# Kernel optimization log

Hardware: AMD Instinct MI355X
Metric: run time of the kernel (lower is better)

Reference implementation:

```python
import jax, jax.numpy as jnp
import numpy as np

NP_, NA_ = 50000, 20000
D_IN, D_HID, D_OUT = 128, 128, 64
E_W, E_C, E_R = 250000, 500000, 250000


def setup_inputs() -> dict:
    key = jax.random.key(0)
    ks = jax.random.split(key, 14)
    s_in = 1.0 / np.sqrt(D_IN)
    s_h = 1.0 / np.sqrt(D_HID)
    return {
        "x_paper": jax.random.normal(ks[0], (NP_, D_IN), jnp.float32),
        "x_author": jax.random.normal(ks[1], (NA_, D_IN), jnp.float32),
        "Wl1": jax.random.normal(ks[2], (3, D_HID, D_IN), jnp.float32) * s_in,
        "bl1": jax.random.normal(ks[3], (3, D_HID), jnp.float32) * 0.01,
        "Wr1": jax.random.normal(ks[4], (3, D_HID, D_IN), jnp.float32) * s_in,
        "Wl2": jax.random.normal(ks[5], (3, D_OUT, D_HID), jnp.float32) * s_h,
        "bl2": jax.random.normal(ks[6], (3, D_OUT), jnp.float32) * 0.01,
        "Wr2": jax.random.normal(ks[7], (3, D_OUT, D_HID), jnp.float32) * s_h,
        "writes_src": jax.random.randint(ks[8], (E_W,), 0, NA_),
        "writes_dst": jax.random.randint(ks[9], (E_W,), 0, NP_),
        "cites_src": jax.random.randint(ks[10], (E_C,), 0, NP_),
        "cites_dst": jax.random.randint(ks[11], (E_C,), 0, NP_),
        "rev_src": jax.random.randint(ks[12], (E_R,), 0, NP_),
        "rev_dst": jax.random.randint(ks[13], (E_R,), 0, NA_),
    }


def _sage(x_src, x_dst, src, dst, Wl, bl, Wr, n_dst):
    # PyG SAGEConv(aggr='mean'): lin_l(mean_j x_src[j]) + lin_r(x_dst)
    agg = jax.ops.segment_sum(x_src[src], dst, num_segments=n_dst)
    cnt = jax.ops.segment_sum(jnp.ones_like(dst, dtype=x_src.dtype), dst,
                              num_segments=n_dst)
    agg = agg / jnp.maximum(cnt, 1.0)[:, None]  # degree-0 nodes -> 0 (PyG scatter-mean)
    return agg @ Wl.T + bl + x_dst @ Wr.T


def reference(x_paper, x_author, Wl1, bl1, Wr1, Wl2, bl2, Wr2,
              writes_src, writes_dst, cites_src, cites_dst, rev_src, rev_dst):
    def hetero_layer(xp, xa, Wl, bl, Wr):
        # HeteroConv(aggr='mean'): average per-relation outputs per dst node type
        op = 0.5 * (_sage(xa, xp, writes_src, writes_dst, Wl[0], bl[0], Wr[0], NP_)
                    + _sage(xp, xp, cites_src, cites_dst, Wl[1], bl[1], Wr[1], NP_))
        oa = _sage(xp, xa, rev_src, rev_dst, Wl[2], bl[2], Wr[2], NA_)
        return op, oa

    hp, ha = hetero_layer(x_paper, x_author, Wl1, bl1, Wr1)
    hp, ha = jax.nn.relu(hp), jax.nn.relu(ha)  # norm_type='none', dropout eval-mode
    hp, _ = hetero_layer(hp, ha, Wl2, bl2, Wr2)
    return hp  # logits for category='paper', [NP_, D_OUT]
```

## Files before the change

kernel.cpp:

```cpp
#include <hip/hip_runtime.h>

#define NP 50000
#define NA 20000
#define E_W 250000
#define E_C 500000
#define E_R 250000
#define E_TOT (E_W + E_C + E_R)
#define CAP 48
#define RBLK 4096
#define NSEG 245
#define PNODES 15000
#define CHK 500
#define NCH 30
#define NBIN 240

typedef __attribute__((ext_vector_type(8))) short short8;
typedef __attribute__((ext_vector_type(4))) float floatx4;
typedef __attribute__((ext_vector_type(2))) float floatx2;

__device__ __forceinline__ unsigned short f2bf(float f) {
    unsigned u = __float_as_uint(f);
    return (unsigned short)((u + 0x7FFFu + ((u >> 16) & 1u)) >> 16);
}
__device__ __forceinline__ float bflo(unsigned v) { return __uint_as_float(v << 16); }
__device__ __forceinline__ float bfhi(unsigned v) { return __uint_as_float(v & 0xFFFF0000u); }

__device__ __forceinline__ int node_idx(int node) {
    if (node < 2 * NP) {
        int rel1 = node >= NP;
        int d = node - (rel1 ? NP : 0);
        int p2 = d / 6250;
        return p2 * PNODES + (d - p2 * 6250) + (rel1 ? 6250 : 0);
    }
    int d = node - 2 * NP;
    int p2 = d / 2500;
    return p2 * PNODES + 12500 + (d - p2 * 2500);
}

__device__ __forceinline__ int frag_off(int NT, int j, int n, int k) {
    int t = n >> 4, ln = n & 15;
    int kb = k >> 5, q = (k >> 3) & 3, r = k & 7;
    return (((j * NT + t) * 4 + kb) * 64 + q * 16 + ln) * 8 + r;
}

__device__ __forceinline__ void prep_body(
    int idx,
    const float* __restrict__ xp, const float* __restrict__ xa,
    const float* __restrict__ Wl1, const float* __restrict__ Wr1,
    const float* __restrict__ Wl2, const float* __restrict__ Wr2,
    const float* __restrict__ bl1, const float* __restrict__ bl2,
    unsigned short* __restrict__ xpb, unsigned short* __restrict__ xab,
    unsigned* __restrict__ xp8, unsigned* __restrict__ xa8,
    unsigned short* __restrict__ Wp1, unsigned short* __restrict__ Wa1,
    unsigned short* __restrict__ Wt2, unsigned short* __restrict__ Wr2s,
    float* __restrict__ bias_p1, float* __restrict__ bias_a1,
    float* __restrict__ bias_p2) {
    const int n4p = NP * 32, n4a = NA * 32;
    if (idx < n4p + n4a) {
        const float* s; unsigned short* d; unsigned* d8; int i = idx;
        if (i < n4p) { s = xp; d = xpb; d8 = xp8; }
        else { s = xa; d = xab; d8 = xa8; i -= n4p; }
        float4 v = ((const float4*)s)[i];
        ushort4 u;
        u.x = f2bf(v.x); u.y = f2bf(v.y); u.z = f2bf(v.z); u.w = f2bf(v.w);
        ((ushort4*)d)[i] = u;
        int w = __builtin_amdgcn_cvt_pk_fp8_f32(v.x, v.y, 0, false);
        w = __builtin_amdgcn_cvt_pk_fp8_f32(v.z, v.w, w, true);
        d8[i] = (unsigned)w;
        return;
    }
    int j = idx - (n4p + n4a);
    if (j < 49152) {
        int jj = j >> 14, rem = j & 16383, n = rem >> 7, k = rem & 127;
        float v = (jj == 0)   ? 0.5f * Wl1[rem]
                  : (jj == 1) ? 0.5f * Wl1[16384 + rem]
                              : 0.5f * (Wr1[rem] + Wr1[16384 + rem]);
        Wp1[frag_off(8, jj, n, k)] = f2bf(v);
    } else if (j < 81920) {
        int i2 = j - 49152;
        int jj = i2 >> 14, rem = i2 & 16383, n = rem >> 7, k = rem & 127;
        float v = (jj == 0) ? Wl1[2 * 16384 + rem] : Wr1[2 * 16384 + rem];
        Wa1[frag_off(8, jj, n, k)] = f2bf(v);
    } else if (j < 98304) {
        int i2 = j - 81920;
        int jj = i2 >> 13, rem = i2 & 8191, n = rem >> 7, k = rem & 127;
        float v = 0.5f * Wl2[jj * 8192 + rem];
        Wt2[frag_off(4, jj, n, k)] = f2bf(v);
    } else if (j < 106496) {
        int i2 = j - 98304;
        int n = i2 >> 7, k = i2 & 127;
        float v = 0.5f * (Wr2[i2] + Wr2[8192 + i2]);
        Wr2s[frag_off(4, 0, n, k)] = f2bf(v);
    } else if (j < 106496 + 320) {
        int b = j - 106496;
        if (b < 128) bias_p1[b] = 0.5f * (bl1[b] + bl1[128 + b]);
        else if (b < 256) bias_a1[b - 128] = bl1[256 + b - 128];
        else bias_p2[b - 256] = 0.5f * (bl2[b - 256] + bl2[64 + b - 256]);
    }
}

__device__ __forceinline__ void edge_bin(
    int e, const int* __restrict__ w_src, const int* __restrict__ w_dst,
    const int* __restrict__ c_src, const int* __restrict__ c_dst,
    const int* __restrict__ r_src, const int* __restrict__ r_dst,
    int& bin, int& sub, int& src) {
    bool isC = (e >= E_W) & (e < E_W + E_C);
    bool isR = e >= E_W + E_C;
    const int* db = isR ? r_dst : (isC ? c_dst : w_dst);
    const int* sb = isR ? r_src : (isC ? c_src : w_src);
    int idx = e - (isC ? E_W : 0) - (isR ? (E_W + E_C) : 0);
    int d = db[idx];
    src = sb[idx];
    int p, local;
    if (isR) { p = d / 2500; local = 12500 + d - p * 2500; }
    else { p = d / 6250; local = (d - p * 6250) + (isC ? 6250 : 0); }
    int ch = local / CHK;
    bin = p * NCH + ch;
    sub = local - ch * CHK;
}

__device__ __forceinline__ void route_body(
    int bid, const int* __restrict__ w_src, const int* __restrict__ w_dst,
    const int* __restrict__ c_src, const int* __restrict__ c_dst,
    const int* __restrict__ r_src, const int* __restrict__ r_dst,
    unsigned* __restrict__ seg, int* __restrict__ segoff, int* __restrict__ segcnt,
    int* cnt_s, int* base_s, int* cur_s) {
    int tid = threadIdx.x, lane = tid & 63;
    for (int k = tid; k < NBIN; k += 256) cnt_s[k] = 0;
    __syncthreads();
#pragma unroll 4
    for (int u = 0; u < 16; ++u) {
        int e = bid * RBLK + u * 256 + tid;
        if (e < E_TOT) {
            int bin, sub, src;
            edge_bin(e, w_src, w_dst, c_src, c_dst, r_src, r_dst, bin, sub, src);
            atomicAdd(&cnt_s[bin], 1);
        }
    }
    __syncthreads();
    if (tid < 64) {
        int v[4], tot = 0;
#pragma unroll
        for (int q = 0; q < 4; ++q) {
            int k = tid * 4 + q;
            v[q] = (k < NBIN) ? cnt_s[k] : 0;
            tot += v[q];
        }
        int sc = tot;
#pragma unroll
        for (int ofs = 1; ofs < 64; ofs <<= 1) {
            int t = __shfl_up(sc, ofs, 64);
            if (lane >= ofs) sc += t;
        }
        int run = sc - tot;
#pragma unroll
        for (int q = 0; q < 4; ++q) {
            int k = tid * 4 + q;
            if (k < NBIN) { base_s[k] = run; run += v[q]; }
        }
    }
    __syncthreads();
    for (int k = tid; k < NBIN; k += 256) {
        segoff[bid * NBIN + k] = base_s[k];
        segcnt[bid * NBIN + k] = cnt_s[k];
        cur_s[k] = base_s[k];
    }
    __syncthreads();
    unsigned* segb = seg + (size_t)bid * RBLK;
#pragma unroll 4
    for (int u = 0; u < 16; ++u) {
        int e = bid * RBLK + u * 256 + tid;
        if (e < E_TOT) {
            int bin, sub, src;
            edge_bin(e, w_src, w_dst, c_src, c_dst, r_src, r_dst, bin, sub, src);
            int pos = atomicAdd(&cur_s[bin], 1);
            segb[pos] = (unsigned)src | ((unsigned)sub << 16);
        }
    }
}

__global__ __launch_bounds__(256) void route_prep(
    const float* xp, const float* xa, const float* Wl1, const float* Wr1,
    const float* Wl2, const float* Wr2, const float* bl1, const float* bl2,
    unsigned short* xpb, unsigned short* xab, unsigned* xp8, unsigned* xa8,
    unsigned short* Wp1, unsigned short* Wa1, unsigned short* Wt2, unsigned short* Wr2s,
    float* bias_p1, float* bias_a1, float* bias_p2,
    const int* w_src, const int* w_dst, const int* c_src, const int* c_dst,
    const int* r_src, const int* r_dst,
    unsigned* seg, int* segoff, int* segcnt) {
    __shared__ int cnt_s[NBIN], base_s[NBIN], cur_s[NBIN];
    if ((int)blockIdx.x < NSEG)
        route_body(blockIdx.x, w_src, w_dst, c_src, c_dst, r_src, r_dst,
                   seg, segoff, segcnt, cnt_s, base_s, cur_s);
    else
        prep_body((blockIdx.x - NSEG) * 256 + threadIdx.x, xp, xa, Wl1, Wr1, Wl2, Wr2,
                  bl1, bl2, xpb, xab, xp8, xa8, Wp1, Wa1, Wt2, Wr2s,
                  bias_p1, bias_a1, bias_p2);
}

__global__ __launch_bounds__(256) void fill2c(
    const unsigned* __restrict__ seg, const int* __restrict__ segoff,
    const int* __restrict__ segcnt, int* __restrict__ cnt,
    unsigned short* __restrict__ csr) {
    __shared__ unsigned short rows[CHK * CAP];
    __shared__ int cursor[CHK];
    __shared__ int offs[NSEG], cnts[NSEG];
    int k = blockIdx.x, tid = threadIdx.x;
    for (int s = tid; s < NSEG; s += 256) {
        offs[s] = segoff[s * NBIN + k];
        cnts[s] = segcnt[s * NBIN + k];
    }
    for (int l = tid; l < CHK; l += 256) cursor[l] = 0;
    __syncthreads();
    int grp = tid >> 4, gl = tid & 15;
    for (int s = grp; s < NSEG; s += 16) {
        int n = cnts[s];
        const unsigned* sp = seg + (size_t)s * RBLK + offs[s];
        for (int i = gl; i < n; i += 16) {
            unsigned v = sp[i];
            int sub = v >> 16, src = v & 0xFFFFu;
            int pos = atomicAdd(&cursor[sub], 1);
            if (pos < CAP) rows[sub * CAP + pos] = (unsigned short)src;
        }
    }
    __syncthreads();
    int p = k / NCH, ch = k - p * NCH;
    int gbase = p * PNODES + ch * CHK;
    for (int l = tid; l < CHK; l += 256) cnt[gbase + l] = cursor[l];
    const unsigned* rU = (const unsigned*)rows;
    unsigned* cU = (unsigned*)csr + (size_t)gbase * (CAP / 2);
    for (int i = tid; i < CHK * (CAP / 2); i += 256) cU[i] = rU[i];
}

__global__ void agg_pad(const unsigned* __restrict__ s0, unsigned short* __restrict__ d0,
                        const unsigned* __restrict__ s1, unsigned short* __restrict__ d1,
                        const unsigned* __restrict__ s2, unsigned short* __restrict__ d2,
                        const int* __restrict__ cnt, const unsigned short* __restrict__ csr) {
    int g = blockIdx.x * 8 + (threadIdx.x >> 5);
    int lane = threadIdx.x & 63;
    int sl = lane & 31, hw = lane & 32;
    const unsigned* sp; unsigned short* dst; int node, dummy;
    if (g < NP) { sp = s0; dst = d0; node = g; dummy = NA; }
    else if (g < 2 * NP) { sp = s1; dst = d1; node = g - NP; dummy = NP; }
    else if (g < 2 * NP + NA) { sp = s2; dst = d2; node = g - 2 * NP; dummy = NP; }
    else return;
    int idx = node_idx(g);
    int deg = cnt[idx];
    int degc = deg < CAP ? deg : CAP;
    const unsigned short* row = csr + (size_t)idx * CAP;
    int ei0 = (sl < degc) ? (int)row[sl] : dummy;
    int ei1 = (32 + sl < degc) ? (int)row[32 + sl] : dummy;
    int degw = degc;
    int other = __shfl_xor(degw, 32, 64);
    if (other > degw) degw = other;
    float a0 = 0.f, a1 = 0.f, a2 = 0.f, a3 = 0.f;
    float b0 = 0.f, b1 = 0.f, b2 = 0.f, b3 = 0.f;
    for (int i = 0; i < degw; i += 8) {
        unsigned v[8];
#pragma unroll
        for (int u = 0; u < 8; ++u) {
            int ii = i + u;
            int esrc = (ii < 32) ? ei0 : ei1;
            int qq = __shfl(esrc, hw | (ii & 31), 64);
            qq = (ii < degc) ? qq : dummy;
            v[u] = sp[(size_t)qq * 32 + sl];
        }
#pragma unroll
        for (int u = 0; u < 8; ++u) {
            floatx2 lo = __builtin_amdgcn_cvt_pk_f32_fp8(v[u], false);
            floatx2 hi = __builtin_amdgcn_cvt_pk_f32_fp8(v[u], true);
            if (u & 1) { b0 += lo.x; b1 += lo.y; b2 += hi.x; b3 += hi.y; }
            else       { a0 += lo.x; a1 += lo.y; a2 += hi.x; a3 += hi.y; }
        }
    }
    float scl = deg > 0 ? 1.f / (float)deg : 0.f;
    float r0 = (a0 + b0) * scl, r1 = (a1 + b1) * scl;
    float r2 = (a2 + b2) * scl, r3 = (a3 + b3) * scl;
    unsigned wlo = ((unsigned)f2bf(r1) << 16) | (unsigned)f2bf(r0);
    unsigned whi = ((unsigned)f2bf(r3) << 16) | (unsigned)f2bf(r2);
    ((uint2*)dst)[(size_t)node * 32 + sl] = make_uint2(wlo, whi);
}

__global__ void agg2(const unsigned short* __restrict__ ta, const unsigned short* __restrict__ tp,
                     const int* __restrict__ cnt, const unsigned short* __restrict__ csr,
                     const float* __restrict__ sp_in, const float* __restrict__ bias_p2,
                     float* __restrict__ out) {
    int node = blockIdx.x * 8 + (threadIdx.x >> 5);
    if (node >= NP) return;
    int lane = threadIdx.x & 63;
    int sl = lane & 31;
    int hw = lane & 32;
    int p2 = node / 6250;
    int base = p2 * PNODES + (node - p2 * 6250);
    float r0 = 0.f, r1 = 0.f;
#pragma unroll
    for (int rel = 0; rel < 2; ++rel) {
        int dummy = (rel == 0) ? NA : NP;
        const unsigned* sp = (const unsigned*)((rel == 0) ? ta : tp);
        int idx = base + (rel ? 6250 : 0);
        int deg = cnt[idx];
        int degc = deg < CAP ? deg : CAP;
        const unsigned short* row = csr + (size_t)idx * CAP;
        int ei0 = (sl < degc) ? (int)row[sl] : dummy;
        int ei1 = (32 + sl < degc) ? (int)row[32 + sl] : dummy;
        int degw = degc;
        int other = __shfl_xor(degw, 32, 64);
        if (other > degw) degw = other;
        float s0 = 0.f, s1 = 0.f, t0 = 0.f, t1 = 0.f;
        for (int i = 0; i < degw; i += 8) {
            unsigned v[8];
#pragma unroll
            for (int u = 0; u < 8; ++u) {
                int ii = i + u;
                int esrc = (ii < 32) ? ei0 : ei1;
                int qq = __shfl(esrc, hw | (ii & 31), 64);
                qq = (ii < degc) ? qq : dummy;
                v[u] = sp[(size_t)qq * 32 + sl];
            }
#pragma unroll
            for (int u = 0; u < 8; ++u) {
                if (u & 1) { t0 += bflo(v[u]); t1 += bfhi(v[u]); }
                else       { s0 += bflo(v[u]); s1 += bfhi(v[u]); }
            }
        }
        float scl = deg > 0 ? 1.f / (float)deg : 0.f;
        r0 += (s0 + t0) * scl; r1 += (s1 + t1) * scl;
    }
    float2 spv = ((const float2*)sp_in)[(size_t)node * 32 + sl];
    float2 bv = ((const float2*)bias_p2)[sl];
    ((float2*)out)[(size_t)node * 32 + sl] =
        make_float2(r0 + spv.x + bv.x, r1 + spv.y + bv.y);
}

template <int J, bool SP>
__device__ __forceinline__ void l1_core(
    const unsigned short* __restrict__ A0, const unsigned short* __restrict__ A1,
    const unsigned short* __restrict__ A2, const unsigned short* __restrict__ Wf,
    const float* __restrict__ bias,
    const unsigned short* __restrict__ Wt, unsigned short* __restrict__ tout,
    const unsigned short* __restrict__ Wsp, float* __restrict__ spout,
    unsigned short (*hT)[136], int M, int blk) {
    int tid = threadIdx.x;
    int wave = tid >> 6, lane = tid & 63;
    int ln = lane & 15, quad = lane >> 4;
    int row = blk * 64 + wave * 16 + ln;
    int rowc = row < M ? row : M - 1;
    const unsigned short* As[3] = {A0, A1, A2};
    floatx4 acc[8];
#pragma unroll
    for (int t = 0; t < 8; ++t) acc[t] = (floatx4){0.f, 0.f, 0.f, 0.f};
#pragma unroll
    for (int j = 0; j < J; ++j) {
        const unsigned short* A = As[j] + (long)rowc * 128 + quad * 8;
        const unsigned short* Wj = Wf + j * (128 * 128) + lane * 8;
#pragma unroll
        for (int kb = 0; kb < 4; ++kb) {
            short8 af = *(const short8*)(A + kb * 32);
#pragma unroll
            for (int t = 0; t < 8; ++t) {
                short8 bf = *(const short8*)(Wj + (t * 4 + kb) * 512);
                acc[t] = __builtin_amdgcn_mfma_f32_16x16x32_bf16(af, bf, acc[t], 0, 0, 0);
            }
        }
    }
    int orow0 = blk * 64 + wave * 16 + quad * 4;
    int lrow0 = wave * 16 + quad * 4;
#pragma unroll
    for (int t = 0; t < 8; ++t) {
        int col = t * 16 + ln;
        float bv = bias[col];
#pragma unroll
        for (int r = 0; r < 4; ++r) {
            float v = fmaxf(acc[t][r] + bv, 0.f);
            hT[lrow0 + r][col] = f2bf(v);
        }
    }
    __syncthreads();
    floatx4 tacc[4], sacc[4];
#pragma unroll
    for (int t = 0; t < 4; ++t) {
        tacc[t] = (floatx4){0.f, 0.f, 0.f, 0.f};
        sacc[t] = (floatx4){0.f, 0.f, 0.f, 0.f};
    }
#pragma unroll
    for (int kb = 0; kb < 4; ++kb) {
        short8 af = *(const short8*)&hT[wave * 16 + ln][quad * 8 + kb * 32];
#pragma unroll
        for (int t = 0; t < 4; ++t) {
            short8 bf = *(const short8*)(Wt + (t * 4 + kb) * 512 + lane * 8);
            tacc[t] = __builtin_amdgcn_mfma_f32_16x16x32_bf16(af, bf, tacc[t], 0, 0, 0);
            if (SP) {
                short8 bs = *(const short8*)(Wsp + (t * 4 + kb) * 512 + lane * 8);
                sacc[t] = __builtin_amdgcn_mfma_f32_16x16x32_bf16(af, bs, sacc[t], 0, 0, 0);
            }
        }
    }
#pragma unroll
    for (int t = 0; t < 4; ++t) {
        int col = t * 16 + ln;
#pragma unroll
        for (int r = 0; r < 4; ++r) {
            int orow = orow0 + r;
            if (orow < M) {
                tout[(long)orow * 64 + col] = f2bf(tacc[t][r]);
                if (SP) spout[(long)orow * 64 + col] = sacc[t][r];
            }
        }
    }
}

__global__ __launch_bounds__(256) void gemm_l1f(
    const unsigned short* aggP1, const unsigned short* aggP2, const unsigned short* xpb,
    const unsigned short* Wp1, const float* bias_p1,
    const unsigned short* aggA, const unsigned short* xab,
    const unsigned short* Wa1, const float* bias_a1,
    const unsigned short* Wt2, const unsigned short* Wr2s,
    unsigned short* ta, unsigned short* tp, float* sp) {
    __shared__ unsigned short hT[64][136];
    constexpr int PB = (NP + 63) / 64;
    if ((int)blockIdx.x < PB)
        l1_core<3, true>(aggP1, aggP2, xpb, Wp1, bias_p1, Wt2 + 64 * 128, tp, Wr2s, sp,
                         hT, NP, blockIdx.x);
    else
        l1_core<2, false>(aggA, xab, nullptr, Wa1, bias_a1, Wt2, ta, nullptr, nullptr,
                          hT, NA, blockIdx.x - PB);
}

extern "C" void kernel_launch(void* const* d_in, const int* in_sizes, int n_in,
                              void* d_out, int out_size, void* d_ws, size_t ws_size,
                              hipStream_t stream) {
    (void)in_sizes; (void)n_in; (void)out_size; (void)ws_size;
    const float* xp  = (const float*)d_in[0];
    const float* xa  = (const float*)d_in[1];
    const float* Wl1 = (const float*)d_in[2];
    const float* bl1 = (const float*)d_in[3];
    const float* Wr1 = (const float*)d_in[4];
    const float* Wl2 = (const float*)d_in[5];
    const float* bl2 = (const float*)d_in[6];
    const float* Wr2 = (const float*)d_in[7];
    const int* w_src = (const int*)d_in[8];
    const int* w_dst = (const int*)d_in[9];
    const int* c_src = (const int*)d_in[10];
    const int* c_dst = (const int*)d_in[11];
    const int* r_src = (const int*)d_in[12];
    const int* r_dst = (const int*)d_in[13];
    float* out = (float*)d_out;

    char* p = (char*)d_ws;
    auto alloc = [&](size_t bytes) {
        char* r = p;
        p += (bytes + 255) & ~(size_t)255;
        return r;
    };
    unsigned short* xpb   = (unsigned short*)alloc((size_t)NP * 128 * 2);
    unsigned short* xab   = (unsigned short*)alloc((size_t)NA * 128 * 2);
    unsigned*       xp8   = (unsigned*)alloc((size_t)(NP + 1) * 128);
    unsigned*       xa8   = (unsigned*)alloc((size_t)(NA + 1) * 128);
    unsigned short* aggP1 = (unsigned short*)alloc((size_t)NP * 128 * 2);
    unsigned short* aggP2 = (unsigned short*)alloc((size_t)NP * 128 * 2);
    unsigned short* aggA  = (unsigned short*)alloc((size_t)NA * 128 * 2);
    unsigned short* ta    = (unsigned short*)alloc((size_t)(NA + 1) * 64 * 2);
    unsigned short* tp    = (unsigned short*)alloc((size_t)(NP + 1) * 64 * 2);
    float*          sp    = (float*)alloc((size_t)NP * 64 * 4);
    int*            cnt    = (int*)alloc((size_t)8 * PNODES * 4);
    unsigned short* csr    = (unsigned short*)alloc((size_t)8 * PNODES * CAP * 2);
    unsigned*       seg    = (unsigned*)alloc((size_t)NSEG * RBLK * 4);
    int*            segoff = (int*)alloc((size_t)NSEG * NBIN * 4);
    int*            segcnt = (int*)alloc((size_t)NSEG * NBIN * 4);
    unsigned short* Wp1  = (unsigned short*)alloc(3 * 128 * 128 * 2);
    unsigned short* Wa1  = (unsigned short*)alloc(2 * 128 * 128 * 2);
    unsigned short* Wt2  = (unsigned short*)alloc(2 * 64 * 128 * 2);
    unsigned short* Wr2s = (unsigned short*)alloc(64 * 128 * 2);
    float* bias_p1 = (float*)alloc(128 * 4);
    float* bias_a1 = (float*)alloc(128 * 4);
    float* bias_p2 = (float*)alloc(64 * 4);

    hipMemsetAsync(xp8 + (size_t)NP * 32, 0, 128, stream);
    hipMemsetAsync(xa8 + (size_t)NA * 32, 0, 128, stream);
    hipMemsetAsync(ta + (size_t)NA * 64, 0, 128, stream);
    hipMemsetAsync(tp + (size_t)NP * 64, 0, 128, stream);

    int prep_threads = (NP + NA) * 32 + 106496 + 320;
    int prep_blocks = (prep_threads + 255) / 256;
    route_prep<<<NSEG + prep_blocks, 256, 0, stream>>>(
        xp, xa, Wl1, Wr1, Wl2, Wr2, bl1, bl2,
        xpb, xab, xp8, xa8, Wp1, Wa1, Wt2, Wr2s, bias_p1, bias_a1, bias_p2,
        w_src, w_dst, c_src, c_dst, r_src, r_dst, seg, segoff, segcnt);

    fill2c<<<NBIN, 256, 0, stream>>>(seg, segoff, segcnt, cnt, csr);

    agg_pad<<<(2 * NP + NA + 7) / 8, 256, 0, stream>>>(xa8, aggP1, xp8, aggP2, xp8, aggA,
                                                       cnt, csr);

    gemm_l1f<<<(NP + 63) / 64 + (NA + 63) / 64, 256, 0, stream>>>(
        aggP1, aggP2, xpb, Wp1, bias_p1, aggA, xab, Wa1, bias_a1, Wt2, Wr2s, ta, tp, sp);

    agg2<<<(NP + 7) / 8, 256, 0, stream>>>(ta, tp, cnt, csr, sp, bias_p2, out);
}
```

Baseline: 219.0 us.

## Split layer-1 GEMM output columns across waves and fold pad memsets into prep

```diff
diff --git a/kernel.cpp b/kernel.cpp
--- a/kernel.cpp
+++ b/kernel.cpp
@@ -54,7 +54,8 @@
     unsigned short* __restrict__ Wp1, unsigned short* __restrict__ Wa1,
     unsigned short* __restrict__ Wt2, unsigned short* __restrict__ Wr2s,
     float* __restrict__ bias_p1, float* __restrict__ bias_a1,
-    float* __restrict__ bias_p2) {
+    float* __restrict__ bias_p2,
+    unsigned short* __restrict__ ta, unsigned short* __restrict__ tp) {
     const int n4p = NP * 32, n4a = NA * 32;
     if (idx < n4p + n4a) {
         const float* s; unsigned short* d; unsigned* d8; int i = idx;
@@ -96,6 +97,12 @@
         if (b < 128) bias_p1[b] = 0.5f * (bl1[b] + bl1[128 + b]);
         else if (b < 256) bias_a1[b - 128] = bl1[256 + b - 128];
         else bias_p2[b - 256] = 0.5f * (bl2[b - 256] + bl2[64 + b - 256]);
+    } else if (j < 106496 + 320 + 128) {
+        int b = j - 106496 - 320;
+        if (b < 32) xp8[(size_t)NP * 32 + b] = 0;
+        else if (b < 64) xa8[(size_t)NA * 32 + (b - 32)] = 0;
+        else if (b < 96) ((unsigned*)ta)[(size_t)NA * 32 + (b - 64)] = 0;
+        else ((unsigned*)tp)[(size_t)NP * 32 + (b - 96)] = 0;
     }
 }
 
@@ -185,6 +192,7 @@
     unsigned short* xpb, unsigned short* xab, unsigned* xp8, unsigned* xa8,
     unsigned short* Wp1, unsigned short* Wa1, unsigned short* Wt2, unsigned short* Wr2s,
     float* bias_p1, float* bias_a1, float* bias_p2,
+    unsigned short* ta, unsigned short* tp,
     const int* w_src, const int* w_dst, const int* c_src, const int* c_dst,
     const int* r_src, const int* r_dst,
     unsigned* seg, int* segoff, int* segcnt) {
@@ -195,7 +203,7 @@
     else
         prep_body((blockIdx.x - NSEG) * 256 + threadIdx.x, xp, xa, Wl1, Wr1, Wl2, Wr2,
                   bl1, bl2, xpb, xab, xp8, xa8, Wp1, Wa1, Wt2, Wr2s,
-                  bias_p1, bias_a1, bias_p2);
+                  bias_p1, bias_a1, bias_p2, ta, tp);
 }
 
 __global__ __launch_bounds__(256) void fill2c(
@@ -343,67 +351,74 @@
     int tid = threadIdx.x;
     int wave = tid >> 6, lane = tid & 63;
     int ln = lane & 15, quad = lane >> 4;
-    int row = blk * 64 + wave * 16 + ln;
-    int rowc = row < M ? row : M - 1;
+    int rowc[4];
+#pragma unroll
+    for (int rg = 0; rg < 4; ++rg) {
+        int row = blk * 64 + rg * 16 + ln;
+        rowc[rg] = row < M ? row : M - 1;
+    }
     const unsigned short* As[3] = {A0, A1, A2};
-    floatx4 acc[8];
-#pragma unroll
-    for (int t = 0; t < 8; ++t) acc[t] = (floatx4){0.f, 0.f, 0.f, 0.f};
+    floatx4 acc[4][2];
+#pragma unroll
+    for (int rg = 0; rg < 4; ++rg)
+#pragma unroll
+        for (int nt = 0; nt < 2; ++nt) acc[rg][nt] = (floatx4){0.f, 0.f, 0.f, 0.f};
 #pragma unroll
     for (int j = 0; j < J; ++j) {
-        const unsigned short* A = As[j] + (long)rowc * 128 + quad * 8;
+        const unsigned short* A = As[j];
         const unsigned short* Wj = Wf + j * (128 * 128) + lane * 8;
 #pragma unroll
         for (int kb = 0; kb < 4; ++kb) {
-            short8 af = *(const short8*)(A + kb * 32);
-#pragma unroll
-            for (int t = 0; t < 8; ++t) {
-                short8 bf = *(const short8*)(Wj + (t * 4 + kb) * 512);
-                acc[t] = __builtin_amdgcn_mfma_f32_16x16x32_bf16(af, bf, acc[t], 0, 0, 0);
+            short8 bf0 = *(const short8*)(Wj + ((wave * 2 + 0) * 4 + kb) * 512);
+            short8 bf1 = *(const short8*)(Wj + ((wave * 2 + 1) * 4 + kb) * 512);
+#pragma unroll
+            for (int rg = 0; rg < 4; ++rg) {
+                short8 af = *(const short8*)(A + (long)rowc[rg] * 128 + quad * 8 + kb * 32);
+                acc[rg][0] = __builtin_amdgcn_mfma_f32_16x16x32_bf16(af, bf0, acc[rg][0], 0, 0, 0);
+                acc[rg][1] = __builtin_amdgcn_mfma_f32_16x16x32_bf16(af, bf1, acc[rg][1], 0, 0, 0);
             }
         }
     }
-    int orow0 = blk * 64 + wave * 16 + quad * 4;
-    int lrow0 = wave * 16 + quad * 4;
-#pragma unroll
-    for (int t = 0; t < 8; ++t) {
-        int col = t * 16 + ln;
-        float bv = bias[col];
+#pragma unroll
+    for (int rg = 0; rg < 4; ++rg)
+#pragma unroll
+        for (int nt = 0; nt < 2; ++nt) {
+            int col = (wave * 2 + nt) * 16 + ln;
+            float bv = bias[col];
+#pragma unroll
+            for (int r = 0; r < 4; ++r) {
+                float v = fmaxf(acc[rg][nt][r] + bv, 0.f);
+                hT[rg * 16 + quad * 4 + r][col] = f2bf(v);
+            }
+        }
+    __syncthreads();
+    floatx4 tacc[4], sacc[4];
+#pragma unroll
+    for (int rg = 0; rg < 4; ++rg) {
+        tacc[rg] = (floatx4){0.f, 0.f, 0.f, 0.f};
+        sacc[rg] = (floatx4){0.f, 0.f, 0.f, 0.f};
+    }
+#pragma unroll
+    for (int kb = 0; kb < 4; ++kb) {
+        short8 bf = *(const short8*)(Wt + (wave * 4 + kb) * 512 + lane * 8);
+        short8 bs;
+        if (SP) bs = *(const short8*)(Wsp + (wave * 4 + kb) * 512 + lane * 8);
+#pragma unroll
+        for (int rg = 0; rg < 4; ++rg) {
+            short8 af = *(const short8*)&hT[rg * 16 + ln][quad * 8 + kb * 32];
+            tacc[rg] = __builtin_amdgcn_mfma_f32_16x16x32_bf16(af, bf, tacc[rg], 0, 0, 0);
+            if (SP) sacc[rg] = __builtin_amdgcn_mfma_f32_16x16x32_bf16(af, bs, sacc[rg], 0, 0, 0);
+        }
+    }
+#pragma unroll
+    for (int rg = 0; rg < 4; ++rg) {
+        int col = wave * 16 + ln;
 #pragma unroll
         for (int r = 0; r < 4; ++r) {
-            float v = fmaxf(acc[t][r] + bv, 0.f);
-            hT[lrow0 + r][col] = f2bf(v);
-        }
-    }
-    __syncthreads();
-    floatx4 tacc[4], sacc[4];
-#pragma unroll
-    for (int t = 0; t < 4; ++t) {
-        tacc[t] = (floatx4){0.f, 0.f, 0.f, 0.f};
-        sacc[t] = (floatx4){0.f, 0.f, 0.f, 0.f};
-    }
-#pragma unroll
-    for (int kb = 0; kb < 4; ++kb) {
-        short8 af = *(const short8*)&hT[wave * 16 + ln][quad * 8 + kb * 32];
-#pragma unroll
-        for (int t = 0; t < 4; ++t) {
-            short8 bf = *(const short8*)(Wt + (t * 4 + kb) * 512 + lane * 8);
-            tacc[t] = __builtin_amdgcn_mfma_f32_16x16x32_bf16(af, bf, tacc[t], 0, 0, 0);
-            if (SP) {
-                short8 bs = *(const short8*)(Wsp + (t * 4 + kb) * 512 + lane * 8);
-                sacc[t] = __builtin_amdgcn_mfma_f32_16x16x32_bf16(af, bs, sacc[t], 0, 0, 0);
-            }
-        }
-    }
-#pragma unroll
-    for (int t = 0; t < 4; ++t) {
-        int col = t * 16 + ln;
-#pragma unroll
-        for (int r = 0; r < 4; ++r) {
-            int orow = orow0 + r;
+            int orow = blk * 64 + rg * 16 + quad * 4 + r;
             if (orow < M) {
-                tout[(long)orow * 64 + col] = f2bf(tacc[t][r]);
-                if (SP) spout[(long)orow * 64 + col] = sacc[t][r];
+                tout[(long)orow * 64 + col] = f2bf(tacc[rg][r]);
+                if (SP) spout[(long)orow * 64 + col] = sacc[rg][r];
             }
         }
     }
@@ -475,16 +490,11 @@
     float* bias_a1 = (float*)alloc(128 * 4);
     float* bias_p2 = (float*)alloc(64 * 4);
 
-    hipMemsetAsync(xp8 + (size_t)NP * 32, 0, 128, stream);
-    hipMemsetAsync(xa8 + (size_t)NA * 32, 0, 128, stream);
-    hipMemsetAsync(ta + (size_t)NA * 64, 0, 128, stream);
-    hipMemsetAsync(tp + (size_t)NP * 64, 0, 128, stream);
-
-    int prep_threads = (NP + NA) * 32 + 106496 + 320;
+    int prep_threads = (NP + NA) * 32 + 106496 + 320 + 128;
     int prep_blocks = (prep_threads + 255) / 256;
     route_prep<<<NSEG + prep_blocks, 256, 0, stream>>>(
         xp, xa, Wl1, Wr1, Wl2, Wr2, bl1, bl2,
-        xpb, xab, xp8, xa8, Wp1, Wa1, Wt2, Wr2s, bias_p1, bias_a1, bias_p2,
+        xpb, xab, xp8, xa8, Wp1, Wa1, Wt2, Wr2s, bias_p1, bias_a1, bias_p2, ta, tp,
         w_src, w_dst, c_src, c_dst, r_src, r_dst, seg, segoff, segcnt);
 
     fill2c<<<NBIN, 256, 0, stream>>>(seg, segoff, segcnt, cnt, csr);
```

Result: no change. 220.7 us (+0.8%).
